# Performance work log

Measured on AMD Instinct MI355X. Metric: run time of the kernel, lower is better.

## Reference

```python
import jax, jax.numpy as jnp
import numpy as np

B, N, T = 2, 512, 4096
D_MODEL, N_MODES, NODE_H, EDGE_H = 128, 32, 128, 256


def _lin(key, d_in, d_out, scale=0.02):
    kw, kb = jax.random.split(key)
    W = jax.random.normal(kw, (d_in, d_out), jnp.float32) * scale
    b = jax.random.normal(kb, (d_out,), jnp.float32) * scale
    return W, b


def setup_inputs() -> dict:
    key = jax.random.key(0)
    ks = jax.random.split(key, 12)
    spikes = jax.random.normal(ks[0], (B, N, T), jnp.float32)
    # temporal FNO spectral weights (init * 0.01 as in torch)
    Wr = jax.random.normal(ks[1], (N_MODES, D_MODEL), jnp.float32) * 0.01
    Wi = jax.random.normal(ks[2], (N_MODES, D_MODEL), jnp.float32) * 0.01
    pw1, pb1 = _lin(ks[3], D_MODEL, D_MODEL)
    pw2, pb2 = _lin(ks[4], D_MODEL, D_MODEL)
    nw1, nb1 = _lin(ks[5], D_MODEL, NODE_H)
    nw2, nb2 = _lin(ks[6], NODE_H, D_MODEL)
    sw, sb = _lin(ks[7], D_MODEL, EDGE_H)
    tw, tb = _lin(ks[8], D_MODEL, EDGE_H)
    ew1, eb1 = _lin(ks[9], 2 * EDGE_H, EDGE_H)
    ew2, eb2 = _lin(ks[10], EDGE_H, EDGE_H // 2)
    ew3, eb3 = _lin(ks[11], EDGE_H // 2, 2)
    alpha = jnp.asarray(1.0, jnp.float32)
    beta = jnp.asarray(0.0, jnp.float32)
    return dict(spikes=spikes, Wr=Wr, Wi=Wi, pw1=pw1, pb1=pb1, pw2=pw2, pb2=pb2,
                nw1=nw1, nb1=nb1, nw2=nw2, nb2=nb2, sw=sw, sb=sb, tw=tw, tb=tb,
                ew1=ew1, eb1=eb1, ew2=ew2, eb2=eb2, ew3=ew3, eb3=eb3,
                alpha=alpha, beta=beta)


def reference(spikes, Wr, Wi, pw1, pb1, pw2, pb2, nw1, nb1, nw2, nb2,
              sw, sb, tw, tb, ew1, eb1, ew2, eb2, ew3, eb3, alpha, beta):
    relu = jax.nn.relu
    # --- TemporalFourierOperator1D ---
    xf = jnp.fft.rfft(spikes, axis=-1)[..., :N_MODES]          # [B,N,K] complex
    xr, xi = xf.real.astype(spikes.dtype), xf.imag.astype(spikes.dtype)
    # broadcast complex multiply: [B,N,K,1] x [K,D] -> [B,N,K,D]
    yr = xr[..., None] * Wr - xi[..., None] * Wi
    yi = xr[..., None] * Wi + xi[..., None] * Wr
    E = jnp.sqrt(yr * yr + yi * yi + 1e-8).mean(axis=2)         # [B,N,D]
    E = relu(E @ pw1 + pb1) @ pw2 + pb2                          # post_mlp
    # --- NodeFeatureNet ---
    H = relu(relu(E @ nw1 + nb1) @ nw2 + nb2)                    # [B,N,D]
    # --- EdgeFourierCoeffNet ---
    hs = H @ sw + sb                                             # [B,N,Eh]
    ht = H @ tw + tb
    # concat([hs,ht]) @ ew1 == hs @ ew1[:Eh] + ht @ ew1[Eh:] (exact same math)
    ps = hs @ ew1[:EDGE_H]                                       # [B,N,Eh]
    pt = ht @ ew1[EDGE_H:]
    h = relu(ps[:, :, None, :] + pt[:, None, :, :] + eb1)        # [B,N,N,Eh]
    h = relu(h @ ew2 + eb2)                                      # [B,N,N,Eh/2]
    rt = h @ ew3 + eb3                                           # [B,N,N,2]
    coeffs = rt[..., 0] + 1j * rt[..., 1]                        # [B,N,N] complex
    # --- AdjacencyLinearDecoder2D ---
    adj_spatial = jnp.fft.ifft2(coeffs, axes=(-2, -1)).real
    adj_logits = alpha * adj_spatial + beta
    adj_prob = jax.nn.sigmoid(adj_logits)
    return adj_logits, adj_prob
```

## Files before the change

kernel.cpp:

```cpp
#include <hip/hip_runtime.h>
#include <hip/hip_bf16.h>
#include <math.h>

typedef __attribute__((ext_vector_type(8))) short short8;
typedef __attribute__((ext_vector_type(8))) _Float16 f16x8;
typedef __attribute__((ext_vector_type(4))) float f32x4;

__device__ __forceinline__ short f2bf(float x) {
    union { float f; unsigned u; } v; v.f = x;
    unsigned r = v.u + 0x7fffu + ((v.u >> 16) & 1u);
    return (short)(r >> 16);
}
__device__ __forceinline__ unsigned cvtpk(float lo, float hi) {
    unsigned r;
    asm("v_cvt_pk_bf16_f32 %0, %1, %2" : "=v"(r) : "v"(lo), "v"(hi));
    return r;
}
__device__ __forceinline__ unsigned pk_addrelu(unsigned a, unsigned b) {
    unsigned r;
    asm("v_pk_add_f16 %0, %1, %2\n\tv_pk_max_f16 %0, %0, 0"
        : "=v"(r) : "v"(a), "v"(b));
    return r;
}
union U32x4 { unsigned u[4]; short8 s8; };
union U32x4H { unsigned u[4]; f16x8 h8; };

__global__ __launch_bounds__(256) void setup_kernel(const float* __restrict__ ew2,
                                                    const float* __restrict__ pw1, const float* __restrict__ pw2,
                                                    const float* __restrict__ nw1, const float* __restrict__ nw2,
                                                    const float* __restrict__ sw, const float* __restrict__ tw,
                                                    const float* __restrict__ sb, const float* __restrict__ tb,
                                                    const float* __restrict__ ew1, const float* __restrict__ eb1,
                                                    short* __restrict__ W4P, short* __restrict__ F1P,
                                                    short* __restrict__ F2, _Float16* __restrict__ EW2H,
                                                    short* __restrict__ PWP,
                                                    short* __restrict__ WCP, float* __restrict__ BC) {
    __shared__ float2 tab[4096];
    __shared__ float eL2[256][32];
    int blk = blockIdx.x, tid = threadIdx.x;
    if (blk < 32) {
        for (int i = tid; i < 4096; i += 256) {
            float sn, cs; sincospif((float)i * (1.0f / 2048.0f), &sn, &cs);
            tab[i] = make_float2(cs, sn);
        }
        __syncthreads();
        int base = blk * 8192;
        #pragma unroll 4
        for (int u = 0; u < 32; ++u) {
            int i = base + u * 256 + tid;
            int j = i & 7, lane = (i >> 3) & 63, nf = (i >> 9) & 3, kkg = i >> 11;
            int k = kkg * 32 + (lane >> 4) * 8 + j;
            int n = nf * 16 + (lane & 15);
            float2 cs = tab[(k * (n & 31)) & 4095];
            W4P[i] = f2bf(n < 32 ? cs.x : -cs.y);
        }
    } else if (blk < 288) {
        for (int i = tid; i < 512; i += 256) {
            float sn, cs; sincospif((float)i * (1.0f / 256.0f), &sn, &cs);
            tab[i] = make_float2(cs, sn);
        }
        __syncthreads();
        int base = (blk - 32) * 4096;
        #pragma unroll 4
        for (int u = 0; u < 16; ++u) {
            int ii = base + u * 256 + tid;
            int j = ii & 7, lane = (ii >> 3) & 63, nfg = (ii >> 9) & 63, kk = ii >> 15;
            int k2 = kk * 32 + (lane >> 4) * 8 + j;
            int t = k2 >> 1, c = k2 & 1;
            int n = nfg * 16 + (lane & 15);
            int q = n >> 1, d = n & 1;
            float2 cs = tab[(t * q) & 511];
            F1P[ii] = f2bf((c == d) ? cs.x : (c ? -cs.y : cs.y));
        }
    } else if (blk < 416) {
        for (int i = tid; i < 512; i += 256) {
            float sn, cs; sincospif((float)i * (1.0f / 256.0f), &sn, &cs);
            tab[i] = make_float2(cs, sn);
        }
        __syncthreads();
        int base = (blk - 288) * 4096;
        #pragma unroll 4
        for (int u = 0; u < 16; ++u) {
            int ii = base + u * 256 + tid;
            int p = ii >> 10, k2 = ii & 1023;
            int s = k2 >> 1, dd = k2 & 1;
            float2 cs = tab[(p * s) & 511];
            F2[ii] = f2bf(dd ? -cs.y : cs.x);
        }
    } else if (blk < 440) {
        int base = (blk - 416) * 4096;
        #pragma unroll 4
        for (int u = 0; u < 16; ++u) {
            int ii = base + u * 256 + tid;
            if (ii < 32768) {
                int j = ii & 7, lane = (ii >> 3) & 63, hf = (ii >> 9) & 7, kk = ii >> 12;
                int k = kk * 32 + (lane >> 4) * 8 + j;
                int h = hf * 16 + (lane & 15);
                EW2H[ii] = (_Float16)ew2[k * 128 + h];
            } else {
                int iw = ii - 32768;
                int l = iw >> 14;
                int r = iw & 16383;
                int j = r & 7, lane = (r >> 3) & 63, nf = (r >> 9) & 7, kk = r >> 12;
                int k = kk * 32 + (lane >> 4) * 8 + j;
                int n = nf * 16 + (lane & 15);
                const float* W = (l == 0) ? pw1 : (l == 1) ? pw2 : (l == 2) ? nw1 : nw2;
                PWP[iw] = f2bf(W[k * 128 + n]);
            }
        }
    } else {
        int blk2 = blk - 440;
        int half = blk2 >> 3, jt = blk2 & 7, j0 = jt * 32;
        const float* ebase = ew1 + (size_t)half * 256 * 256;
        for (int it = 0; it < 32; ++it) {
            int idx = tid + it * 256;
            int i = idx >> 5, jj = idx & 31;
            eL2[i][jj] = ebase[(size_t)i * 256 + j0 + jj];
        }
        __syncthreads();
        const float* wp = half ? tw : sw;
        int d = tid >> 1, jh = tid & 1;
        float acc[16];
        #pragma unroll
        for (int x = 0; x < 16; ++x) acc[x] = 0.f;
        #pragma unroll 4
        for (int i = 0; i < 256; ++i) {
            float wv = wp[(size_t)d * 256 + i];
            #pragma unroll
            for (int x = 0; x < 16; ++x) acc[x] += wv * eL2[i][jh * 16 + x];
        }
        int kk = d >> 5, lg = (d >> 3) & 3, j = d & 7;
        #pragma unroll
        for (int x = 0; x < 16; ++x) {
            int n = half * 256 + j0 + jh * 16 + x;
            int lane = lg * 16 + (n & 15);
            WCP[((kk * 32 + (n >> 4)) * 64 + lane) * 8 + j] = f2bf(acc[x]);
        }
        if (tid < 32) {
            const float* bv = half ? tb : sb;
            float a = 0.f;
            #pragma unroll 8
            for (int i = 0; i < 256; ++i) a += bv[i] * eL2[i][tid];
            if (half == 0) a += eb1[j0 + tid];
            BC[half * 256 + j0 + tid] = a;
        }
    }
}

__global__ __launch_bounds__(256) void dft_mfma(const float* __restrict__ spikes,
                                                const short* __restrict__ W4P,
                                                float* __restrict__ X64P) {
    __shared__ float red[4][4][64][4];
    int part = blockIdx.x & 7;
    int row0 = (blockIdx.x >> 3) * 16;
    int tid = threadIdx.x, wid = tid >> 6, lane = tid & 63;
    int lrow = lane & 15, lg = lane >> 4;

    f32x4 acc[4];
    #pragma unroll
    for (int n = 0; n < 4; ++n) acc[n] = (f32x4){0.f, 0.f, 0.f, 0.f};

    int row = row0 + lrow;
    const float* sbase = spikes + (size_t)row * 4096;
    #pragma unroll
    for (int kk = 0; kk < 4; ++kk) {
        int k = part * 512 + wid * 128 + kk * 32 + lg * 8;
        const float4* sp = (const float4*)(sbase + k);
        float4 v0 = sp[0], v1 = sp[1];
        U32x4 a;
        a.u[0] = cvtpk(v0.x, v0.y);
        a.u[1] = cvtpk(v0.z, v0.w);
        a.u[2] = cvtpk(v1.x, v1.y);
        a.u[3] = cvtpk(v1.z, v1.w);
        int kkg = part * 16 + wid * 4 + kk;
        #pragma unroll
        for (int n = 0; n < 4; ++n) {
            short8 bfr = *(const short8*)(W4P + ((kkg * 4 + n) * 64 + lane) * 8);
            acc[n] = __builtin_amdgcn_mfma_f32_16x16x32_bf16(a.s8, bfr, acc[n], 0, 0, 0);
        }
    }
    #pragma unroll
    for (int n = 0; n < 4; ++n)
        #pragma unroll
        for (int r = 0; r < 4; ++r) red[wid][n][lane][r] = acc[n][r];
    __syncthreads();
    #pragma unroll
    for (int r = 0; r < 4; ++r) {
        float s = red[0][wid][lane][r] + red[1][wid][lane][r]
                + red[2][wid][lane][r] + red[3][wid][lane][r];
        int orow = row0 + lg * 4 + r;
        X64P[(size_t)part * 65536 + (size_t)orow * 64 + wid * 16 + lrow] = s;
    }
}

__global__ __launch_bounds__(512) void k_node(const float* __restrict__ X64P,
                                              const float* __restrict__ Wr, const float* __restrict__ Wi,
                                              const short* __restrict__ PWP,
                                              const float* __restrict__ pb1, const float* __restrict__ pb2,
                                              const float* __restrict__ nb1, const float* __restrict__ nb2,
                                              const short* __restrict__ WCP, const float* __restrict__ BC,
                                              _Float16* __restrict__ PS16, _Float16* __restrict__ PT16) {
    __shared__ float sx[8][64];
    __shared__ float wri[8192];
    __shared__ short abuf[16 * 128];
    int r0 = blockIdx.x * 8, tid = threadIdx.x;
    int wid = tid >> 6, lane = tid & 63;
    int lrow = lane & 15, lg = lane >> 4;

    {
        int row = tid >> 6, col = tid & 63;
        float v = 0.f;
        #pragma unroll
        for (int p = 0; p < 8; ++p)
            v += X64P[(size_t)p * 65536 + (size_t)(r0 + row) * 64 + col];
        sx[row][col] = v;
    }
    #pragma unroll
    for (int it = 0; it < 16; ++it) {
        int idx = tid + it * 512;
        wri[idx] = (idx < 4096) ? Wr[idx] : Wi[idx - 4096];
    }
    abuf[1024 + tid] = 0;
    abuf[1536 + tid] = 0;
    __syncthreads();

    #pragma unroll
    for (int it = 0; it < 2; ++it) {
        int idx = tid + it * 512;
        int row = idx >> 7, d = idx & 127;
        float acc = 0.f;
        #pragma unroll 8
        for (int k = 0; k < 32; ++k) {
            float a = sx[row][k], b = sx[row][32 + k];
            float wr = wri[k * 128 + d], wi = wri[4096 + k * 128 + d];
            float yr = a * wr - b * wi;
            float yi = a * wi + b * wr;
            acc += sqrtf(yr * yr + yi * yi + 1e-8f);
        }
        abuf[row * 128 + (d ^ ((row & 7) << 3))] = f2bf(acc * (1.0f / 32.0f));
    }
    __syncthreads();

    int asw = (lrow & 7) << 3;
    #pragma unroll 1
    for (int l = 0; l < 4; ++l) {
        f32x4 acc2 = (f32x4){0.f, 0.f, 0.f, 0.f};
        #pragma unroll
        for (int kk = 0; kk < 4; ++kk) {
            short8 a = *(const short8*)(abuf + lrow * 128 + ((kk * 32 + lg * 8) ^ asw));
            short8 b = *(const short8*)(PWP + (((l * 4 + kk) * 8 + wid) * 64 + lane) * 8);
            acc2 = __builtin_amdgcn_mfma_f32_16x16x32_bf16(a, b, acc2, 0, 0, 0);
        }
        __syncthreads();
        const float* bp = (l == 0) ? pb1 : (l == 1) ? pb2 : (l == 2) ? nb1 : nb2;
        bool rl = (l != 1);
        int n = wid * 16 + lrow;
        float bv = bp[n];
        #pragma unroll
        for (int r = 0; r < 4; ++r) {
            int orow = lg * 4 + r;
            float v = acc2[r] + bv;
            if (rl) v = fmaxf(v, 0.f);
            abuf[orow * 128 + (n ^ ((orow & 7) << 3))] = f2bf(v);
        }
        __syncthreads();
    }

    f32x4 acc3[4];
    #pragma unroll
    for (int f = 0; f < 4; ++f) acc3[f] = (f32x4){0.f, 0.f, 0.f, 0.f};
    #pragma unroll
    for (int kk = 0; kk < 4; ++kk) {
        short8 a = *(const short8*)(abuf + lrow * 128 + ((kk * 32 + lg * 8) ^ asw));
        #pragma unroll
        for (int f = 0; f < 4; ++f) {
            short8 b = *(const short8*)(WCP + ((kk * 32 + wid * 4 + f) * 64 + lane) * 8);
            acc3[f] = __builtin_amdgcn_mfma_f32_16x16x32_bf16(a, b, acc3[f], 0, 0, 0);
        }
    }
    if (lg < 2) {
        #pragma unroll
        for (int f = 0; f < 4; ++f) {
            int n = (wid * 4 + f) * 16 + lrow;
            float bv = BC[n];
            _Float16* dst = (n < 256) ? (PS16 + n) : (PT16 + (n - 256));
            #pragma unroll
            for (int r = 0; r < 4; ++r) {
                int row = r0 + lg * 4 + r;
                dst[(size_t)row * 256] = (_Float16)(acc3[f][r] + bv);
            }
        }
    }
}

__global__ __launch_bounds__(512, 2) void edge_mfma10(
    const _Float16* __restrict__ PS16, const _Float16* __restrict__ PT16,
    const uint4* __restrict__ EW2H4,
    const float* __restrict__ eb2, const float* __restrict__ ew3,
    const float* __restrict__ eb3, unsigned* __restrict__ CC32) {
    __shared__ __align__(16) unsigned ew2s[8192];
    __shared__ __align__(16) unsigned pts[8192];
    __shared__ __align__(16) unsigned pss[2048];
    __shared__ float eb2s[128];
    __shared__ float ew3s[256];
    __shared__ float part[2][4][64][2];

    int bidx = blockIdx.x;
    int ttile = bidx & 7;
    int stile = (bidx >> 3) & 31;
    int b = bidx >> 8;
    int s0 = stile * 16, t0 = ttile * 64;
    int tid = threadIdx.x;

    { uint4* dst = (uint4*)ew2s;
      #pragma unroll
      for (int it = 0; it < 4; ++it) {
          int idx = tid + it * 512;
          int lane_ = idx & 63;
          int rest = idx >> 6;
          int hfl = rest & 1, hh_ = (rest >> 1) & 1, kk_ = rest >> 2;
          dst[idx] = EW2H4[(size_t)((kk_ * 8 + hh_ * 4 + hfl) * 64 + lane_)];
      } }
    { const uint4* src = (const uint4*)(PT16 + (size_t)(b * 512 + t0) * 256);
      uint4* dst = (uint4*)pts;
      #pragma unroll
      for (int it = 0; it < 4; ++it) {
          int idx = tid + it * 512;
          int t = idx >> 5, g = idx & 31;
          dst[t * 32 + (g ^ (t & 7))] = src[idx];
      } }
    { const uint4* src = (const uint4*)(PS16 + (size_t)(b * 512 + s0) * 256);
      ((uint4*)pss)[tid] = src[tid]; }
    if (tid < 128) eb2s[tid] = eb2[tid];
    if (tid < 256) ew3s[tid] = ew3[tid];
    __syncthreads();

    int wid = tid >> 6, lane = tid & 63;
    int lrow = lane & 15, lg = lane >> 4;
    int hh = wid >> 2;
    int sq = wid & 3;
    float e30 = eb3[0], e31 = eb3[1];
    const uint4* pts4 = (const uint4*)pts;
    const uint4* pss4 = (const uint4*)pss;
    const uint4* ew24 = (const uint4*)ew2s;

    #pragma unroll 1
    for (int i = 0; i < 4; ++i) {
        int s_local = sq * 4 + i;
        int buf = i & 1;

        f32x4 acc[4][4];
        #pragma unroll
        for (int hf = 0; hf < 4; ++hf)
            #pragma unroll
            for (int tf = 0; tf < 4; ++tf) acc[hf][tf] = (f32x4){0.f, 0.f, 0.f, 0.f};

        #pragma unroll
        for (int kk = 0; kk < 8; ++kk) {
            uint4 pA = pss4[s_local * 32 + kk * 4 + lg];
            uint4 av0 = ew24[(kk * 4 + hh * 2 + 0) * 64 + lane];
            uint4 av1 = ew24[(kk * 4 + hh * 2 + 1) * 64 + lane];
            uint4 av2 = EW2H4[(size_t)((kk * 8 + hh * 4 + 2) * 64 + lane)];
            uint4 av3 = EW2H4[(size_t)((kk * 8 + hh * 4 + 3) * 64 + lane)];
            f16x8 bf[4];
            #pragma unroll
            for (int tf = 0; tf < 4; ++tf) {
                int t = tf * 16 + lrow;
                uint4 v = pts4[t * 32 + ((kk * 4 + lg) ^ (t & 7))];
                U32x4H r;
                r.u[0] = pk_addrelu(v.x, pA.x);
                r.u[1] = pk_addrelu(v.y, pA.y);
                r.u[2] = pk_addrelu(v.z, pA.z);
                r.u[3] = pk_addrelu(v.w, pA.w);
                bf[tf] = r.h8;
            }
            __builtin_amdgcn_s_setprio(1);
            #pragma unroll
            for (int hf = 0; hf < 4; ++hf) {
                U32x4H af;
                uint4 av = (hf == 0) ? av0 : (hf == 1) ? av1 : (hf == 2) ? av2 : av3;
                af.u[0] = av.x; af.u[1] = av.y; af.u[2] = av.z; af.u[3] = av.w;
                #pragma unroll
                for (int tf = 0; tf < 4; ++tf)
                    acc[hf][tf] = __builtin_amdgcn_mfma_f32_16x16x32_f16(af.h8, bf[tf], acc[hf][tf], 0, 0, 0);
            }
            __builtin_amdgcn_s_setprio(0);
        }

        float p0[4], p1[4];
        #pragma unroll
        for (int tf = 0; tf < 4; ++tf) {
            float a0 = 0.f, a1 = 0.f;
            #pragma unroll
            for (int hf = 0; hf < 4; ++hf)
                #pragma unroll
                for (int r = 0; r < 4; ++r) {
                    int h = hh * 64 + hf * 16 + lg * 4 + r;
                    float hv = fmaxf(acc[hf][tf][r] + eb2s[h], 0.f);
                    a0 += hv * ew3s[2 * h];
                    a1 += hv * ew3s[2 * h + 1];
                }
            a0 += __shfl_xor(a0, 16); a1 += __shfl_xor(a1, 16);
            a0 += __shfl_xor(a0, 32); a1 += __shfl_xor(a1, 32);
            p0[tf] = a0; p1[tf] = a1;
        }
        if (hh == 1 && lg == 0) {
            #pragma unroll
            for (int tf = 0; tf < 4; ++tf) {
                part[buf][sq][tf * 16 + lrow][0] = p0[tf];
                part[buf][sq][tf * 16 + lrow][1] = p1[tf];
            }
        }
        __syncthreads();
        if (hh == 0 && lg == 0) {
            size_t outrow = (size_t)(b * 512 + s0 + s_local) * 512;
            #pragma unroll
            for (int tf = 0; tf < 4; ++tf) {
                int tl = tf * 16 + lrow;
                float t0v = p0[tf] + part[buf][sq][tl][0] + e30;
                float t1v = p1[tf] + part[buf][sq][tl][1] + e31;
                CC32[outrow + t0 + tl] = cvtpk(t0v, t1v);
            }
        }
    }
}

__global__ __launch_bounds__(256) void ifft1_mfma(const short* __restrict__ CC,
                                                  const short* __restrict__ F1P,
                                                  short* __restrict__ B2P) {
    __shared__ short st[32 * 64];
    int bidx = blockIdx.x;
    int nt = bidx & 7;
    int mt = bidx >> 3;
    int bs0 = mt * 16;
    int b = mt >> 5;
    int kk2 = mt & 31;
    int tid = threadIdx.x, wid = tid >> 6, lane = tid & 63;
    int lrow = lane & 15, lg = lane >> 4;

    f32x4 acc[2];
    acc[0] = (f32x4){0.f, 0.f, 0.f, 0.f};
    acc[1] = (f32x4){0.f, 0.f, 0.f, 0.f};

    const short* arow = CC + (size_t)(bs0 + lrow) * 1024 + lg * 8;
    #pragma unroll 4
    for (int kk = 0; kk < 32; ++kk) {
        short8 a = *(const short8*)(arow + kk * 32);
        #pragma unroll
        for (int f = 0; f < 2; ++f) {
            int nfg = nt * 8 + wid * 2 + f;
            short8 bfr = *(const short8*)(F1P + ((kk * 64 + nfg) * 64 + lane) * 8);
            acc[f] = __builtin_amdgcn_mfma_f32_16x16x32_bf16(a, bfr, acc[f], 0, 0, 0);
        }
    }
    #pragma unroll
    for (int f = 0; f < 2; ++f)
        #pragma unroll
        for (int r = 0; r < 4; ++r) {
            int n_local = (wid * 2 + f) * 16 + lrow;
            int lq = n_local >> 1, d = n_local & 1;
            int lk = (lg * 4 + r) * 2 + d;
            st[lk * 64 + lq] = f2bf(acc[f][r]);
        }
    __syncthreads();
    {
        int f2 = wid;
        int nf2 = nt * 4 + f2;
        short8 v;
        #pragma unroll
        for (int j = 0; j < 8; ++j)
            v[j] = st[((lane >> 4) * 8 + j) * 64 + f2 * 16 + (lane & 15)];
        *(short8*)(B2P + (size_t)b * 524288 + ((size_t)(kk2 * 32 + nf2) * 64 + lane) * 8) = v;
    }
}

__global__ __launch_bounds__(256) void ifft2_mfma(const short* __restrict__ B2P,
                                                  const short* __restrict__ F2,
                                                  const float* __restrict__ alpha, const float* __restrict__ beta,
                                                  float* __restrict__ out) {
    int bidx = blockIdx.x;
    int pt_ = bidx & 31;
    int qt = (bidx >> 5) & 7;
    int b = bidx >> 8;
    int p0 = pt_ * 16;
    int tid = threadIdx.x, wid = tid >> 6, lane = tid & 63;
    int lrow = lane & 15, lg = lane >> 4;

    f32x4 acc = (f32x4){0.f, 0.f, 0.f, 0.f};

    const short* arow = F2 + (size_t)(p0 + lrow) * 1024 + lg * 8;
    const short* bbase = B2P + (size_t)b * 524288;
    int nfg = qt * 4 + wid;
    #pragma unroll 4
    for (int kk = 0; kk < 32; ++kk) {
        short8 a = *(const short8*)(arow + kk * 32);
        short8 bfr = *(const short8*)(bbase + ((size_t)(kk * 32 + nfg) * 64 + lane) * 8);
        acc = __builtin_amdgcn_mfma_f32_16x16x32_bf16(a, bfr, acc, 0, 0, 0);
    }
    float al = alpha[0], be = beta[0];
    const float scale = 1.0f / (512.0f * 512.0f);
    #pragma unroll
    for (int r = 0; r < 4; ++r) {
        int q = qt * 64 + wid * 16 + lrow;
        int p = p0 + lg * 4 + r;
        float l = al * (acc[r] * scale) + be;
        size_t idx = (size_t)b * 262144 + (size_t)p * 512 + q;
        out[idx] = l;
        out[524288 + idx] = 1.f / (1.f + expf(-l));
    }
}

extern "C" void kernel_launch(void* const* d_in, const int* in_sizes, int n_in,
                              void* d_out, int out_size, void* d_ws, size_t ws_size,
                              hipStream_t stream) {
    const float* spikes = (const float*)d_in[0];
    const float* Wr  = (const float*)d_in[1];
    const float* Wi  = (const float*)d_in[2];
    const float* pw1 = (const float*)d_in[3];
    const float* pb1 = (const float*)d_in[4];
    const float* pw2 = (const float*)d_in[5];
    const float* pb2 = (const float*)d_in[6];
    const float* nw1 = (const float*)d_in[7];
    const float* nb1 = (const float*)d_in[8];
    const float* nw2 = (const float*)d_in[9];
    const float* nb2 = (const float*)d_in[10];
    const float* sw  = (const float*)d_in[11];
    const float* sb  = (const float*)d_in[12];
    const float* tw_ = (const float*)d_in[13];
    const float* tb  = (const float*)d_in[14];
    const float* ew1 = (const float*)d_in[15];
    const float* eb1 = (const float*)d_in[16];
    const float* ew2 = (const float*)d_in[17];
    const float* eb2 = (const float*)d_in[18];
    const float* ew3 = (const float*)d_in[19];
    const float* eb3 = (const float*)d_in[20];
    const float* alpha = (const float*)d_in[21];
    const float* beta  = (const float*)d_in[22];
    float* out = (float*)d_out;
    float* ws  = (float*)d_ws;

    unsigned* CC    = (unsigned*)(ws + 0);
    float*    X64P  = ws + 0;
    short*    WCP   = (short*)(ws + 524288);
    float*    BC    = ws + 557056;
    _Float16* PS16  = (_Float16*)(ws + 1048576);
    _Float16* PT16  = (_Float16*)(ws + 1179648);
    short*    B2P   = (short*)(ws + 1048576);
    _Float16* EW2H  = (_Float16*)(ws + 1572864);
    short*    W4P   = (short*)(ws + 1589248);
    short*    F1P   = (short*)(ws + 1720320);
    short*    F2    = (short*)(ws + 2244608);
    short*    PWP   = (short*)(ws + 2506752);

    setup_kernel<<<456, 256, 0, stream>>>(ew2, pw1, pw2, nw1, nw2, sw, tw_, sb, tb, ew1, eb1,
                                          W4P, F1P, F2, EW2H, PWP, WCP, BC);
    dft_mfma<<<512, 256, 0, stream>>>(spikes, W4P, X64P);
    k_node<<<128, 512, 0, stream>>>(X64P, Wr, Wi, PWP, pb1, pb2, nb1, nb2, WCP, BC, PS16, PT16);
    edge_mfma10<<<512, 512, 0, stream>>>(PS16, PT16, (const uint4*)EW2H, eb2, ew3, eb3, CC);
    ifft1_mfma<<<512, 256, 0, stream>>>((const short*)CC, F1P, B2P);
    ifft2_mfma<<<512, 256, 0, stream>>>(B2P, F2, alpha, beta, out);
}
```

Before: 111.6 us.

## Give each edge warp all hidden channels to drop cross-warp partial reduction

The edge MLP kernel changes its work split. Each wave now covers all 128 hidden outputs for two source rows, processed as two 32-wide target halves, instead of two waves splitting the hidden dimension per source row. This removes the shared-memory partial-sum buffer and the per-iteration block barrier. The LDS copy of ew2 now holds hidden fragments 0-3 and 4-7 stream from global/L2. Each wave now issues twice as many A-fragment loads per pA/B computation, but there is no cross-wave sync and the second-layer reduction finishes in registers.

```diff
diff --git a/kernel.cpp b/kernel.cpp
--- a/kernel.cpp
+++ b/kernel.cpp
@@ -293,7 +293,7 @@
     }
 }
 
-__global__ __launch_bounds__(512, 2) void edge_mfma10(
+__global__ __launch_bounds__(512, 2) void edge_mfma11(
     const _Float16* __restrict__ PS16, const _Float16* __restrict__ PT16,
     const uint4* __restrict__ EW2H4,
     const float* __restrict__ eb2, const float* __restrict__ ew3,
@@ -303,7 +303,6 @@
     __shared__ __align__(16) unsigned pss[2048];
     __shared__ float eb2s[128];
     __shared__ float ew3s[256];
-    __shared__ float part[2][4][64][2];
 
     int bidx = blockIdx.x;
     int ttile = bidx & 7;
@@ -318,8 +317,7 @@
           int idx = tid + it * 512;
           int lane_ = idx & 63;
           int rest = idx >> 6;
-          int hfl = rest & 1, hh_ = (rest >> 1) & 1, kk_ = rest >> 2;
-          dst[idx] = EW2H4[(size_t)((kk_ * 8 + hh_ * 4 + hfl) * 64 + lane_)];
+          dst[idx] = EW2H4[(size_t)(((rest >> 2) * 8 + (rest & 3)) * 64 + lane_)];
       } }
     { const uint4* src = (const uint4*)(PT16 + (size_t)(b * 512 + t0) * 256);
       uint4* dst = (uint4*)pts;
@@ -337,89 +335,81 @@
 
     int wid = tid >> 6, lane = tid & 63;
     int lrow = lane & 15, lg = lane >> 4;
-    int hh = wid >> 2;
-    int sq = wid & 3;
     float e30 = eb3[0], e31 = eb3[1];
     const uint4* pts4 = (const uint4*)pts;
     const uint4* pss4 = (const uint4*)pss;
     const uint4* ew24 = (const uint4*)ew2s;
+    const uint4* ew2g = EW2H4 + lane;
 
     #pragma unroll 1
-    for (int i = 0; i < 4; ++i) {
-        int s_local = sq * 4 + i;
-        int buf = i & 1;
-
-        f32x4 acc[4][4];
-        #pragma unroll
-        for (int hf = 0; hf < 4; ++hf)
+    for (int i = 0; i < 2; ++i) {
+        int s_local = wid * 2 + i;
+        #pragma unroll 1
+        for (int tp = 0; tp < 2; ++tp) {
+            f32x4 acc[8][2];
             #pragma unroll
-            for (int tf = 0; tf < 4; ++tf) acc[hf][tf] = (f32x4){0.f, 0.f, 0.f, 0.f};
-
-        #pragma unroll
-        for (int kk = 0; kk < 8; ++kk) {
-            uint4 pA = pss4[s_local * 32 + kk * 4 + lg];
-            uint4 av0 = ew24[(kk * 4 + hh * 2 + 0) * 64 + lane];
-            uint4 av1 = ew24[(kk * 4 + hh * 2 + 1) * 64 + lane];
-            uint4 av2 = EW2H4[(size_t)((kk * 8 + hh * 4 + 2) * 64 + lane)];
-            uint4 av3 = EW2H4[(size_t)((kk * 8 + hh * 4 + 3) * 64 + lane)];
-            f16x8 bf[4];
+            for (int hf = 0; hf < 8; ++hf)
+                #pragma unroll
+                for (int tf = 0; tf < 2; ++tf) acc[hf][tf] = (f32x4){0.f, 0.f, 0.f, 0.f};
+
             #pragma unroll
-            for (int tf = 0; tf < 4; ++tf) {
-                int t = tf * 16 + lrow;
-                uint4 v = pts4[t * 32 + ((kk * 4 + lg) ^ (t & 7))];
-                U32x4H r;
-                r.u[0] = pk_addrelu(v.x, pA.x);
-                r.u[1] = pk_addrelu(v.y, pA.y);
-                r.u[2] = pk_addrelu(v.z, pA.z);
-                r.u[3] = pk_addrelu(v.w, pA.w);
-                bf[tf] = r.h8;
+            for (int kk = 0; kk < 8; ++kk) {
+                uint4 g4 = ew2g[(kk * 8 + 4) * 64];
+                uint4 g5 = ew2g[(kk * 8 + 5) * 64];
+                uint4 g6 = ew2g[(kk * 8 + 6) * 64];
+                uint4 g7 = ew2g[(kk * 8 + 7) * 64];
+                uint4 pA = pss4[s_local * 32 + kk * 4 + lg];
+                f16x8 bf[2];
+                #pragma unroll
+                for (int tf = 0; tf < 2; ++tf) {
+                    int t = tp * 32 + tf * 16 + lrow;
+                    uint4 v = pts4[t * 32 + ((kk * 4 + lg) ^ (t & 7))];
+                    U32x4H r;
+                    r.u[0] = pk_addrelu(v.x, pA.x);
+                    r.u[1] = pk_addrelu(v.y, pA.y);
+                    r.u[2] = pk_addrelu(v.z, pA.z);
+                    r.u[3] = pk_addrelu(v.w, pA.w);
+                    bf[tf] = r.h8;
+                }
+                __builtin_amdgcn_s_setprio(1);
+                #pragma unroll
+                for (int hf = 0; hf < 4; ++hf) {
+                    U32x4H af;
+                    uint4 av = ew24[(kk * 4 + hf) * 64 + lane];
+                    af.u[0] = av.x; af.u[1] = av.y; af.u[2] = av.z; af.u[3] = av.w;
+                    #pragma unroll
+                    for (int tf = 0; tf < 2; ++tf)
+                        acc[hf][tf] = __builtin_amdgcn_mfma_f32_16x16x32_f16(af.h8, bf[tf], acc[hf][tf], 0, 0, 0);
+                }
+                #pragma unroll
+                for (int hf = 4; hf < 8; ++hf) {
+                    U32x4H af;
+                    uint4 av = (hf == 4) ? g4 : (hf == 5) ? g5 : (hf == 6) ? g6 : g7;
+                    af.u[0] = av.x; af.u[1] = av.y; af.u[2] = av.z; af.u[3] = av.w;
+                    #pragma unroll
+                    for (int tf = 0; tf < 2; ++tf)
+                        acc[hf][tf] = __builtin_amdgcn_mfma_f32_16x16x32_f16(af.h8, bf[tf], acc[hf][tf], 0, 0, 0);
+                }
+                __builtin_amdgcn_s_setprio(0);
             }
-            __builtin_amdgcn_s_setprio(1);
-            #pragma unroll
-            for (int hf = 0; hf < 4; ++hf) {
-                U32x4H af;
-                uint4 av = (hf == 0) ? av0 : (hf == 1) ? av1 : (hf == 2) ? av2 : av3;
-                af.u[0] = av.x; af.u[1] = av.y; af.u[2] = av.z; af.u[3] = av.w;
-                #pragma unroll
-                for (int tf = 0; tf < 4; ++tf)
-                    acc[hf][tf] = __builtin_amdgcn_mfma_f32_16x16x32_f16(af.h8, bf[tf], acc[hf][tf], 0, 0, 0);
-            }
-            __builtin_amdgcn_s_setprio(0);
-        }
-
-        float p0[4], p1[4];
-        #pragma unroll
-        for (int tf = 0; tf < 4; ++tf) {
-            float a0 = 0.f, a1 = 0.f;
-            #pragma unroll
-            for (int hf = 0; hf < 4; ++hf)
-                #pragma unroll
-                for (int r = 0; r < 4; ++r) {
-                    int h = hh * 64 + hf * 16 + lg * 4 + r;
-                    float hv = fmaxf(acc[hf][tf][r] + eb2s[h], 0.f);
-                    a0 += hv * ew3s[2 * h];
-                    a1 += hv * ew3s[2 * h + 1];
-                }
-            a0 += __shfl_xor(a0, 16); a1 += __shfl_xor(a1, 16);
-            a0 += __shfl_xor(a0, 32); a1 += __shfl_xor(a1, 32);
-            p0[tf] = a0; p1[tf] = a1;
-        }
-        if (hh == 1 && lg == 0) {
-            #pragma unroll
-            for (int tf = 0; tf < 4; ++tf) {
-                part[buf][sq][tf * 16 + lrow][0] = p0[tf];
-                part[buf][sq][tf * 16 + lrow][1] = p1[tf];
-            }
-        }
-        __syncthreads();
-        if (hh == 0 && lg == 0) {
+
             size_t outrow = (size_t)(b * 512 + s0 + s_local) * 512;
             #pragma unroll
-            for (int tf = 0; tf < 4; ++tf) {
-                int tl = tf * 16 + lrow;
-                float t0v = p0[tf] + part[buf][sq][tl][0] + e30;
-                float t1v = p1[tf] + part[buf][sq][tl][1] + e31;
-                CC32[outrow + t0 + tl] = cvtpk(t0v, t1v);
+            for (int tf = 0; tf < 2; ++tf) {
+                float a0 = 0.f, a1 = 0.f;
+                #pragma unroll
+                for (int hf = 0; hf < 8; ++hf)
+                    #pragma unroll
+                    for (int r = 0; r < 4; ++r) {
+                        int h = hf * 16 + lg * 4 + r;
+                        float hv = fmaxf(acc[hf][tf][r] + eb2s[h], 0.f);
+                        a0 += hv * ew3s[2 * h];
+                        a1 += hv * ew3s[2 * h + 1];
+                    }
+                a0 += __shfl_xor(a0, 16); a1 += __shfl_xor(a1, 16);
+                a0 += __shfl_xor(a0, 32); a1 += __shfl_xor(a1, 32);
+                if (lg == 0)
+                    CC32[outrow + t0 + tp * 32 + tf * 16 + lrow] = cvtpk(a0 + e30, a1 + e31);
             }
         }
     }
@@ -556,7 +546,7 @@
                                           W4P, F1P, F2, EW2H, PWP, WCP, BC);
     dft_mfma<<<512, 256, 0, stream>>>(spikes, W4P, X64P);
     k_node<<<128, 512, 0, stream>>>(X64P, Wr, Wi, PWP, pb1, pb2, nb1, nb2, WCP, BC, PS16, PT16);
-    edge_mfma10<<<512, 512, 0, stream>>>(PS16, PT16, (const uint4*)EW2H, eb2, ew3, eb3, CC);
+    edge_mfma11<<<512, 512, 0, stream>>>(PS16, PT16, (const uint4*)EW2H, eb2, ew3, eb3, CC);
     ifft1_mfma<<<512, 256, 0, stream>>>((const short*)CC, F1P, B2P);
     ifft2_mfma<<<512, 256, 0, stream>>>(B2P, F2, alpha, beta, out);
 }
```

Result: no change. 113.1 us (median of 2 runs) (+1.4%).
